# Kernel tuning notes

Measured on AMD Instinct MI355X. Metric: run time of the kernel, lower is better.

## Reference

```python
import jax, jax.numpy as jnp
import numpy as np

B, L, H, V = 64, 2048, 1024, 50257


def setup_inputs() -> dict:
    key = jax.random.key(0)
    ks = jax.random.split(key, 12)
    s = 0.02
    return {
        "input_seq": jax.random.randint(ks[0], (B,), 0, V),
        "encoder_outputs": jax.random.normal(ks[1], (L, B, H), jnp.float32),
        "h0": jax.random.normal(ks[2], (1, B, H), jnp.float32),
        "c0": jax.random.normal(ks[3], (1, B, H), jnp.float32),
        "emb": jax.random.normal(ks[4], (V, H), jnp.float32) * s,
        "W_ih": jax.random.normal(ks[5], (4 * H, H), jnp.float32) * s,
        "W_hh": jax.random.normal(ks[6], (4 * H, H), jnp.float32) * s,
        "b_ih": jnp.zeros((4 * H,), jnp.float32),
        "b_hh": jnp.zeros((4 * H,), jnp.float32),
        "W_concat": jax.random.normal(ks[7], (H, 2 * H), jnp.float32) * s,
        "b_concat": jnp.zeros((H,), jnp.float32),
        "W_out": jax.random.normal(ks[8], (V, H), jnp.float32) * s,
        "b_out": jnp.zeros((V,), jnp.float32),
    }


def reference(input_seq, encoder_outputs, h0, c0, emb, W_ih, W_hh, b_ih, b_hh,
              W_concat, b_concat, W_out, b_out):
    # Embedding lookup (dropout is identity at eval)
    x = emb[input_seq]                      # [B, H]
    h, c = h0[0], c0[0]                     # [B, H] each (n_layers == 1)

    # Single LSTM step, PyTorch gate order (i, f, g, o)
    gates = x @ W_ih.T + b_ih + h @ W_hh.T + b_hh   # [B, 4H]
    i, f, g, o = jnp.split(gates, 4, axis=-1)
    i, f, o = jax.nn.sigmoid(i), jax.nn.sigmoid(f), jax.nn.sigmoid(o)
    g = jnp.tanh(g)
    c1 = f * c + i * g
    h1 = o * jnp.tanh(c1)                   # rnn_output, [B, H]

    # Luong 'dot' attention: replaces the per-(b,i) python double loop
    energies = jnp.einsum('bh,lbh->bl', h1, encoder_outputs)   # [B, L]
    attn = jax.nn.softmax(energies, axis=1)                    # [B, L]
    context = jnp.einsum('bl,lbh->bh', attn, encoder_outputs)  # [B, H]

    concat_out = jnp.tanh(jnp.concatenate([h1, context], axis=1) @ W_concat.T + b_concat)
    output = concat_out @ W_out.T + b_out                      # [B, V]

    return output, h1[None], c1[None], attn[:, None, :]
```

## Files before the change

kernel.cpp:

```cpp
#include <hip/hip_runtime.h>
#include <math.h>

#define B 64
#define Lw 2048
#define Hd 1024
#define Vd 50257

#define WS_XHB    0
#define WS_CATB   98304
#define WS_ENERGY 163840
#define WS_PART   294912
#define WS_CONC   2408448

#define OUT_H1   3216448
#define OUT_C1   3281984
#define OUT_ATTN 3347520

#define NCHUNK 32
#define LCHUNK 64
#define PSTRIDE 1032

typedef __bf16 bf16x8 __attribute__((ext_vector_type(8)));
typedef float f32x4 __attribute__((ext_vector_type(4)));

__device__ __forceinline__ float sigm(float x) { return 1.f / (1.f + expf(-x)); }

#define CVT8(dst, w0, w1)                                            \
    dst[0] = (__bf16)w0.x; dst[1] = (__bf16)w0.y;                    \
    dst[2] = (__bf16)w0.z; dst[3] = (__bf16)w0.w;                    \
    dst[4] = (__bf16)w1.x; dst[5] = (__bf16)w1.y;                    \
    dst[6] = (__bf16)w1.z; dst[7] = (__bf16)w1.w;

__global__ void k_embed(const int* __restrict__ seq, const float* __restrict__ emb,
                        const float* __restrict__ h0, __bf16* __restrict__ xhb)
{
    int b = blockIdx.x;
    int t = threadIdx.x;
    int tok = seq[b];
    float4 xv = *(const float4*)(emb + (size_t)tok * Hd + t * 4);
    float4 hv = *(const float4*)(h0 + (size_t)b * Hd + t * 4);
    int kb = t >> 1, ko = (t & 1) * 4;
    __bf16* xp = xhb + (size_t)kb * 512 + b * 8 + ko;
    xp[0] = (__bf16)xv.x; xp[1] = (__bf16)xv.y;
    xp[2] = (__bf16)xv.z; xp[3] = (__bf16)xv.w;
    __bf16* hp = xhb + (size_t)(128 + kb) * 512 + b * 8 + ko;
    __bf16* lp = xhb + (size_t)(256 + kb) * 512 + b * 8 + ko;
    float h[4] = {hv.x, hv.y, hv.z, hv.w};
#pragma unroll
    for (int i = 0; i < 4; ++i) {
        __bf16 hi = (__bf16)h[i];
        hp[i] = hi;
        lp[i] = (__bf16)(h[i] - (float)hi);
    }
}

__global__ void k_gates_lstm(const __bf16* __restrict__ xhb,
                             const float* __restrict__ W_ih, const float* __restrict__ W_hh,
                             const float* __restrict__ b_ih, const float* __restrict__ b_hh,
                             const float* __restrict__ c0,
                             float* __restrict__ h1o, float* __restrict__ c1o,
                             __bf16* __restrict__ catb)
{
    __shared__ float lds[8][64][20];
    __shared__ float gsum[16][66];
    int wave = threadIdx.x >> 6, lane = threadIdx.x & 63;
    int hh0 = blockIdx.x * 4;
    int rloc = lane & 15;
    int wrow = (rloc >> 2) * Hd + hh0 + (rloc & 3);
    int kq = lane >> 4;
    int isH = wave >> 2;
    int kbase = (wave & 3) * 256;

    const float* wp = (isH ? W_hh : W_ih) + (size_t)wrow * Hd + kbase + kq * 8;
    const __bf16* apx = xhb + rloc * 8;

    f32x4 acc[4] = {{0.f,0.f,0.f,0.f},{0.f,0.f,0.f,0.f},
                    {0.f,0.f,0.f,0.f},{0.f,0.f,0.f,0.f}};

    if (!isH) {
#pragma unroll 4
        for (int k0 = 0; k0 < 256; k0 += 32) {
            float4 w0 = *(const float4*)(wp + k0);
            float4 w1 = *(const float4*)(wp + k0 + 4);
            bf16x8 bf; CVT8(bf, w0, w1);
            int kb = ((kbase + k0) >> 3) + kq;
#pragma unroll
            for (int mt = 0; mt < 4; ++mt) {
                bf16x8 a = *(const bf16x8*)(apx + (size_t)kb * 512 + mt * 128);
                acc[mt] = __builtin_amdgcn_mfma_f32_16x16x32_bf16(a, bf, acc[mt], 0, 0, 0);
            }
        }
    } else {
#pragma unroll 2
        for (int k0 = 0; k0 < 256; k0 += 32) {
            float4 w0 = *(const float4*)(wp + k0);
            float4 w1 = *(const float4*)(wp + k0 + 4);
            bf16x8 bhi, blo;
            float wf[8] = {w0.x, w0.y, w0.z, w0.w, w1.x, w1.y, w1.z, w1.w};
#pragma unroll
            for (int i = 0; i < 8; ++i) {
                __bf16 hi = (__bf16)wf[i];
                bhi[i] = hi;
                blo[i] = (__bf16)(wf[i] - (float)hi);
            }
            int kb = ((kbase + k0) >> 3) + kq;
#pragma unroll
            for (int mt = 0; mt < 4; ++mt) {
                bf16x8 ahi = *(const bf16x8*)(apx + (size_t)(128 + kb) * 512 + mt * 128);
                bf16x8 alo = *(const bf16x8*)(apx + (size_t)(256 + kb) * 512 + mt * 128);
                acc[mt] = __builtin_amdgcn_mfma_f32_16x16x32_bf16(ahi, bhi, acc[mt], 0, 0, 0);
                acc[mt] = __builtin_amdgcn_mfma_f32_16x16x32_bf16(ahi, blo, acc[mt], 0, 0, 0);
                acc[mt] = __builtin_amdgcn_mfma_f32_16x16x32_bf16(alo, bhi, acc[mt], 0, 0, 0);
            }
        }
    }

#pragma unroll
    for (int mt = 0; mt < 4; ++mt)
        *(f32x4*)&lds[wave][lane][mt * 4] = acc[mt];
    __syncthreads();

    if (wave < 4) {
        int mt = wave;
        float bv = b_ih[wrow] + b_hh[wrow];
#pragma unroll
        for (int r = 0; r < 4; ++r) {
            float s = 0.f;
#pragma unroll
            for (int w = 0; w < 8; ++w) s += lds[w][lane][mt * 4 + r];
            int m = mt * 16 + kq * 4 + r;
            gsum[rloc][m] = s + bv;
        }
    }
    __syncthreads();

    int t = threadIdx.x;
    if (t < 256) {
        int b = t & 63, hl = t >> 6;
        int hh = hh0 + hl;
        float gi = gsum[0 + hl][b];
        float gf = gsum[4 + hl][b];
        float gg = gsum[8 + hl][b];
        float go = gsum[12 + hl][b];
        float c  = c0[(size_t)b * Hd + hh];
        float c1 = sigm(gf) * c + sigm(gi) * tanhf(gg);
        float h1 = sigm(go) * tanhf(c1);
        h1o[(size_t)b * Hd + hh] = h1;
        c1o[(size_t)b * Hd + hh] = c1;
        catb[(size_t)(hh >> 3) * 512 + b * 8 + (hh & 7)] = (__bf16)h1;
    }
}

__global__ void k_attn_part(const float* __restrict__ enc, const float* __restrict__ h1,
                            float* __restrict__ energy, float* __restrict__ part)
{
    int chunk = blockIdx.x, b = blockIdx.y;
    int wave = threadIdx.x >> 6, lane = threadIdx.x & 63;

    float4 qv[4], ctx[4];
#pragma unroll
    for (int q = 0; q < 4; ++q) {
        qv[q] = *(const float4*)(h1 + (size_t)b * Hd + q * 256 + lane * 4);
        ctx[q] = make_float4(0.f, 0.f, 0.f, 0.f);
    }
    float m = -INFINITY, s = 0.f;

    int l0 = chunk * LCHUNK + wave * 2;
    const float* ep0 = enc + ((size_t)l0 * B + b) * Hd + lane * 4;
    const float* ep1 = ep0 + (size_t)B * Hd;
    float4 ev0[4], ev1[4];
#pragma unroll
    for (int q = 0; q < 4; ++q) {
        ev0[q] = *(const float4*)(ep0 + q * 256);
        ev1[q] = *(const float4*)(ep1 + q * 256);
    }

    for (int i = 0; i < LCHUNK / 8; ++i) {
        int l = chunk * LCHUNK + i * 8 + wave * 2;
        int ln = (i < LCHUNK / 8 - 1) ? (l + 8) : l;
        const float* np0 = enc + ((size_t)ln * B + b) * Hd + lane * 4;
        const float* np1 = np0 + (size_t)B * Hd;
        float4 nv0[4], nv1[4];
#pragma unroll
        for (int q = 0; q < 4; ++q) {
            nv0[q] = *(const float4*)(np0 + q * 256);
            nv1[q] = *(const float4*)(np1 + q * 256);
        }

        float d0 = 0.f, d1 = 0.f;
#pragma unroll
        for (int q = 0; q < 4; ++q) {
            d0 += ev0[q].x * qv[q].x + ev0[q].y * qv[q].y
                + ev0[q].z * qv[q].z + ev0[q].w * qv[q].w;
            d1 += ev1[q].x * qv[q].x + ev1[q].y * qv[q].y
                + ev1[q].z * qv[q].z + ev1[q].w * qv[q].w;
        }
#pragma unroll
        for (int off = 32; off >= 1; off >>= 1) {
            d0 += __shfl_xor(d0, off);
            d1 += __shfl_xor(d1, off);
        }
        if (lane == 0) {
            energy[(size_t)b * Lw + l] = d0;
            energy[(size_t)b * Lw + l + 1] = d1;
        }

        float mn = fmaxf(d0, d1);
        if (mn > m) {
            float sc = expf(m - mn);
            s *= sc;
#pragma unroll
            for (int q = 0; q < 4; ++q) {
                ctx[q].x *= sc; ctx[q].y *= sc; ctx[q].z *= sc; ctx[q].w *= sc;
            }
            m = mn;
        }
        float w0 = expf(d0 - m), w1 = expf(d1 - m);
        s += w0 + w1;
#pragma unroll
        for (int q = 0; q < 4; ++q) {
            ctx[q].x += w0 * ev0[q].x + w1 * ev1[q].x;
            ctx[q].y += w0 * ev0[q].y + w1 * ev1[q].y;
            ctx[q].z += w0 * ev0[q].z + w1 * ev1[q].z;
            ctx[q].w += w0 * ev0[q].w + w1 * ev1[q].w;
        }
#pragma unroll
        for (int q = 0; q < 4; ++q) { ev0[q] = nv0[q]; ev1[q] = nv1[q]; }
    }

    __shared__ float lctx[4][Hd];
    __shared__ float lms[4][2];
#pragma unroll
    for (int q = 0; q < 4; ++q)
        *(float4*)(&lctx[wave][q * 256 + lane * 4]) = ctx[q];
    if (lane == 0) { lms[wave][0] = m; lms[wave][1] = s; }
    __syncthreads();

    float mb = fmaxf(fmaxf(lms[0][0], lms[1][0]), fmaxf(lms[2][0], lms[3][0]));
    float sc0 = expf(lms[0][0] - mb), sc1 = expf(lms[1][0] - mb);
    float sc2 = expf(lms[2][0] - mb), sc3 = expf(lms[3][0] - mb);
    float sb = lms[0][1] * sc0 + lms[1][1] * sc1 + lms[2][1] * sc2 + lms[3][1] * sc3;

    int t = threadIdx.x;
    float* pb = part + (size_t)(chunk * B + b) * PSTRIDE;
    float4 a0 = *(float4*)(&lctx[0][t * 4]);
    float4 a1 = *(float4*)(&lctx[1][t * 4]);
    float4 a2 = *(float4*)(&lctx[2][t * 4]);
    float4 a3 = *(float4*)(&lctx[3][t * 4]);
    float4 v;
    v.x = a0.x * sc0 + a1.x * sc1 + a2.x * sc2 + a3.x * sc3;
    v.y = a0.y * sc0 + a1.y * sc1 + a2.y * sc2 + a3.y * sc3;
    v.z = a0.z * sc0 + a1.z * sc1 + a2.z * sc2 + a3.z * sc3;
    v.w = a0.w * sc0 + a1.w * sc1 + a2.w * sc2 + a3.w * sc3;
    *(float4*)(pb + t * 4) = v;
    if (t == 0) { pb[1024] = mb; pb[1025] = sb; }
}

__global__ void k_attn_combine(const float* __restrict__ part,
                               const float* __restrict__ energy,
                               __bf16* __restrict__ catb, float* __restrict__ attn)
{
    int b = blockIdx.x, t = threadIdx.x;
    float m = -INFINITY;
#pragma unroll
    for (int c = 0; c < NCHUNK; ++c)
        m = fmaxf(m, part[(size_t)(c * B + b) * PSTRIDE + 1024]);
    float s = 0.f, scl[NCHUNK];
#pragma unroll
    for (int c = 0; c < NCHUNK; ++c) {
        const float* pb = part + (size_t)(c * B + b) * PSTRIDE;
        scl[c] = expf(pb[1024] - m);
        s += pb[1025] * scl[c];
    }
    float4 v = make_float4(0.f, 0.f, 0.f, 0.f);
#pragma unroll
    for (int c = 0; c < NCHUNK; ++c) {
        float4 p = *(const float4*)(part + (size_t)(c * B + b) * PSTRIDE + t * 4);
        v.x += p.x * scl[c]; v.y += p.y * scl[c]; v.z += p.z * scl[c]; v.w += p.w * scl[c];
    }
    float inv = 1.f / s;
    v.x *= inv; v.y *= inv; v.z *= inv; v.w *= inv;
    int k = 1024 + t * 4;
    __bf16* cp = catb + (size_t)(k >> 3) * 512 + b * 8 + (k & 7);
    cp[0] = (__bf16)v.x; cp[1] = (__bf16)v.y;
    cp[2] = (__bf16)v.z; cp[3] = (__bf16)v.w;

#pragma unroll
    for (int j = 0; j < 8; ++j) {
        int l = t + j * 256;
        attn[(size_t)b * Lw + l] = expf(energy[(size_t)b * Lw + l] - m) * inv;
    }
}

__global__ void k_concat_mfma(const __bf16* __restrict__ catb,
                              const float* __restrict__ W, const float* __restrict__ bias,
                              __bf16* __restrict__ conc)
{
    __shared__ float lds[8][64][20];
    int wave = threadIdx.x >> 6, lane = threadIdx.x & 63;
    int n0 = blockIdx.x * 16;
    int nl = n0 + (lane & 15);
    int kq = lane >> 4;
    int kbase = wave * 256;

    const float* wp = W + (size_t)nl * (2 * Hd) + kbase + kq * 8;
    const __bf16* ap = catb + (lane & 15) * 8;

    f32x4 acc[4] = {{0.f,0.f,0.f,0.f},{0.f,0.f,0.f,0.f},
                    {0.f,0.f,0.f,0.f},{0.f,0.f,0.f,0.f}};

#pragma unroll 4
    for (int k0 = 0; k0 < 256; k0 += 32) {
        float4 w0 = *(const float4*)(wp + k0);
        float4 w1 = *(const float4*)(wp + k0 + 4);
        bf16x8 bf; CVT8(bf, w0, w1);
        int kb = ((kbase + k0) >> 3) + kq;
#pragma unroll
        for (int mt = 0; mt < 4; ++mt) {
            bf16x8 a = *(const bf16x8*)(ap + (size_t)kb * 512 + mt * 128);
            acc[mt] = __builtin_amdgcn_mfma_f32_16x16x32_bf16(a, bf, acc[mt], 0, 0, 0);
        }
    }

#pragma unroll
    for (int mt = 0; mt < 4; ++mt)
        *(f32x4*)&lds[wave][lane][mt * 4] = acc[mt];
    __syncthreads();

    if (wave < 4) {
        int mt = wave;
        float bv = bias[nl];
#pragma unroll
        for (int r = 0; r < 4; ++r) {
            float s = 0.f;
#pragma unroll
            for (int w = 0; w < 8; ++w) s += lds[w][lane][mt * 4 + r];
            int m = mt * 16 + kq * 4 + r;
            conc[(size_t)(nl >> 3) * 512 + m * 8 + (nl & 7)] = (__bf16)tanhf(s + bv);
        }
    }
}

__global__ void k_vocab_mfma(const __bf16* __restrict__ apack,
                             const float* __restrict__ W,
                             const float* __restrict__ bias,
                             float* __restrict__ out)
{
    int wave = threadIdx.x >> 6;
    int lane = threadIdx.x & 63;
    int n0 = (blockIdx.x * 4 + wave) * 16;
    if (n0 > Vd - 16) n0 = Vd - 16;

    int nl = n0 + (lane & 15);
    int kq = lane >> 4;
    const float* wp = W + (size_t)nl * Hd + kq * 8;
    const __bf16* ap = apack + (size_t)(lane & 15) * 8;

    f32x4 acc[4] = {{0.f,0.f,0.f,0.f},{0.f,0.f,0.f,0.f},
                    {0.f,0.f,0.f,0.f},{0.f,0.f,0.f,0.f}};

    float4 c0 = *(const float4*)(wp + 0);
    float4 c1 = *(const float4*)(wp + 4);
    float4 c2 = *(const float4*)(wp + 32);
    float4 c3 = *(const float4*)(wp + 36);

#pragma unroll 2
    for (int k0 = 0; k0 < Hd; k0 += 64) {
        int kn = (k0 + 64 < Hd) ? (k0 + 64) : k0;
        float4 p0 = *(const float4*)(wp + kn);
        float4 p1 = *(const float4*)(wp + kn + 4);
        float4 p2 = *(const float4*)(wp + kn + 32);
        float4 p3 = *(const float4*)(wp + kn + 36);

        bf16x8 bf0; CVT8(bf0, c0, c1);
        bf16x8 bf1; CVT8(bf1, c2, c3);
        int kb0 = (k0 >> 3) + kq, kb1 = kb0 + 4;
#pragma unroll
        for (int mt = 0; mt < 4; ++mt) {
            bf16x8 a0 = *(const bf16x8*)(ap + (size_t)kb0 * 512 + mt * 128);
            acc[mt] = __builtin_amdgcn_mfma_f32_16x16x32_bf16(a0, bf0, acc[mt], 0, 0, 0);
        }
#pragma unroll
        for (int mt = 0; mt < 4; ++mt) {
            bf16x8 a1 = *(const bf16x8*)(ap + (size_t)kb1 * 512 + mt * 128);
            acc[mt] = __builtin_amdgcn_mfma_f32_16x16x32_bf16(a1, bf1, acc[mt], 0, 0, 0);
        }
        c0 = p0; c1 = p1; c2 = p2; c3 = p3;
    }

    float bv = bias[nl];
#pragma unroll
    for (int mt = 0; mt < 4; ++mt)
#pragma unroll
        for (int r = 0; r < 4; ++r) {
            int m = mt * 16 + (lane >> 4) * 4 + r;
            out[(size_t)m * Vd + nl] = acc[mt][r] + bv;
        }
}

extern "C" void kernel_launch(void* const* d_in, const int* in_sizes, int n_in,
                              void* d_out, int out_size, void* d_ws, size_t ws_size,
                              hipStream_t stream)
{
    const int*   seq    = (const int*)d_in[0];
    const float* enc    = (const float*)d_in[1];
    const float* h0     = (const float*)d_in[2];
    const float* c0     = (const float*)d_in[3];
    const float* emb    = (const float*)d_in[4];
    const float* W_ih   = (const float*)d_in[5];
    const float* W_hh   = (const float*)d_in[6];
    const float* b_ih   = (const float*)d_in[7];
    const float* b_hh   = (const float*)d_in[8];
    const float* W_cat  = (const float*)d_in[9];
    const float* b_cat  = (const float*)d_in[10];
    const float* W_out  = (const float*)d_in[11];
    const float* b_out  = (const float*)d_in[12];
    float* out = (float*)d_out;
    float* ws  = (float*)d_ws;

    __bf16* xhb    = (__bf16*)(ws + WS_XHB);
    __bf16* catb   = (__bf16*)(ws + WS_CATB);
    float*  energy = ws + WS_ENERGY;
    float*  part   = ws + WS_PART;
    __bf16* conc   = (__bf16*)(ws + WS_CONC);

    k_embed<<<B, 256, 0, stream>>>(seq, emb, h0, xhb);
    k_gates_lstm<<<256, 512, 0, stream>>>(xhb, W_ih, W_hh, b_ih, b_hh, c0,
                                          out + OUT_H1, out + OUT_C1, catb);
    k_attn_part<<<dim3(NCHUNK, B), 256, 0, stream>>>(enc, out + OUT_H1, energy, part);
    k_attn_combine<<<B, 256, 0, stream>>>(part, energy, catb, out + OUT_ATTN);
    k_concat_mfma<<<64, 512, 0, stream>>>(catb, W_cat, b_cat, conc);
    k_vocab_mfma<<<786, 256, 0, stream>>>(conc, W_out, b_out, out);
}
```

Before: 232.2 us.

## Fuse embedding into LSTM gates, merge attention combine via atomic counter, shrink vocab blocks

Removes the separate embedding kernel: the gates kernel now gathers embedding rows and h0 directly from fp32 and converts or splits them to bf16 in registers. The attention combine kernel is folded into the partial kernel, where the last block per batch row (found with an atomic counter that the gates kernel resets) does the final reduction. The manual register prefetch in the attention loop is dropped, and the vocab GEMM switches to 128-thread blocks with twice as many blocks. This saves two launches, but the gates kernel now repeats conversions and global gathers, and dropping the prefetch may expose more memory latency.

Measured after the change: 781.3 us. 237% more time.

```diff
diff --git a/kernel.cpp b/kernel.cpp
--- a/kernel.cpp
+++ b/kernel.cpp
@@ -6,11 +6,11 @@
 #define Hd 1024
 #define Vd 50257
 
-#define WS_XHB    0
-#define WS_CATB   98304
-#define WS_ENERGY 163840
-#define WS_PART   294912
-#define WS_CONC   2408448
+#define WS_CATB   0
+#define WS_ENERGY 65536
+#define WS_PART   196608
+#define WS_CNT    2310144
+#define WS_CONC   2310272
 
 #define OUT_H1   3216448
 #define OUT_C1   3281984
@@ -31,38 +31,19 @@
     dst[4] = (__bf16)w1.x; dst[5] = (__bf16)w1.y;                    \
     dst[6] = (__bf16)w1.z; dst[7] = (__bf16)w1.w;
 
-__global__ void k_embed(const int* __restrict__ seq, const float* __restrict__ emb,
-                        const float* __restrict__ h0, __bf16* __restrict__ xhb)
-{
-    int b = blockIdx.x;
-    int t = threadIdx.x;
-    int tok = seq[b];
-    float4 xv = *(const float4*)(emb + (size_t)tok * Hd + t * 4);
-    float4 hv = *(const float4*)(h0 + (size_t)b * Hd + t * 4);
-    int kb = t >> 1, ko = (t & 1) * 4;
-    __bf16* xp = xhb + (size_t)kb * 512 + b * 8 + ko;
-    xp[0] = (__bf16)xv.x; xp[1] = (__bf16)xv.y;
-    xp[2] = (__bf16)xv.z; xp[3] = (__bf16)xv.w;
-    __bf16* hp = xhb + (size_t)(128 + kb) * 512 + b * 8 + ko;
-    __bf16* lp = xhb + (size_t)(256 + kb) * 512 + b * 8 + ko;
-    float h[4] = {hv.x, hv.y, hv.z, hv.w};
-#pragma unroll
-    for (int i = 0; i < 4; ++i) {
-        __bf16 hi = (__bf16)h[i];
-        hp[i] = hi;
-        lp[i] = (__bf16)(h[i] - (float)hi);
-    }
-}
-
-__global__ void k_gates_lstm(const __bf16* __restrict__ xhb,
+__global__ void k_gates_lstm(const int* __restrict__ seq,
+                             const float* __restrict__ emb, const float* __restrict__ h0,
                              const float* __restrict__ W_ih, const float* __restrict__ W_hh,
                              const float* __restrict__ b_ih, const float* __restrict__ b_hh,
                              const float* __restrict__ c0,
                              float* __restrict__ h1o, float* __restrict__ c1o,
-                             __bf16* __restrict__ catb)
+                             __bf16* __restrict__ catb, int* __restrict__ cnt)
 {
     __shared__ float lds[8][64][20];
     __shared__ float gsum[16][66];
+
+    if (blockIdx.x == 0 && threadIdx.x < 64) cnt[threadIdx.x] = 0;
+
     int wave = threadIdx.x >> 6, lane = threadIdx.x & 63;
     int hh0 = blockIdx.x * 4;
     int rloc = lane & 15;
@@ -72,22 +53,26 @@
     int kbase = (wave & 3) * 256;
 
     const float* wp = (isH ? W_hh : W_ih) + (size_t)wrow * Hd + kbase + kq * 8;
-    const __bf16* apx = xhb + rloc * 8;
 
     f32x4 acc[4] = {{0.f,0.f,0.f,0.f},{0.f,0.f,0.f,0.f},
                     {0.f,0.f,0.f,0.f},{0.f,0.f,0.f,0.f}};
 
     if (!isH) {
-#pragma unroll 4
+        int tok[4];
+#pragma unroll
+        for (int mt = 0; mt < 4; ++mt) tok[mt] = seq[mt * 16 + rloc];
+#pragma unroll 2
         for (int k0 = 0; k0 < 256; k0 += 32) {
             float4 w0 = *(const float4*)(wp + k0);
             float4 w1 = *(const float4*)(wp + k0 + 4);
             bf16x8 bf; CVT8(bf, w0, w1);
-            int kb = ((kbase + k0) >> 3) + kq;
 #pragma unroll
             for (int mt = 0; mt < 4; ++mt) {
-                bf16x8 a = *(const bf16x8*)(apx + (size_t)kb * 512 + mt * 128);
-                acc[mt] = __builtin_amdgcn_mfma_f32_16x16x32_bf16(a, bf, acc[mt], 0, 0, 0);
+                const float* xp = emb + (size_t)tok[mt] * Hd + kbase + k0 + kq * 8;
+                float4 a0 = *(const float4*)xp;
+                float4 a1 = *(const float4*)(xp + 4);
+                bf16x8 af; CVT8(af, a0, a1);
+                acc[mt] = __builtin_amdgcn_mfma_f32_16x16x32_bf16(af, bf, acc[mt], 0, 0, 0);
             }
         }
     } else {
@@ -96,18 +81,28 @@
             float4 w0 = *(const float4*)(wp + k0);
             float4 w1 = *(const float4*)(wp + k0 + 4);
             bf16x8 bhi, blo;
-            float wf[8] = {w0.x, w0.y, w0.z, w0.w, w1.x, w1.y, w1.z, w1.w};
-#pragma unroll
-            for (int i = 0; i < 8; ++i) {
-                __bf16 hi = (__bf16)wf[i];
-                bhi[i] = hi;
-                blo[i] = (__bf16)(wf[i] - (float)hi);
+            {
+                float wf[8] = {w0.x, w0.y, w0.z, w0.w, w1.x, w1.y, w1.z, w1.w};
+#pragma unroll
+                for (int i = 0; i < 8; ++i) {
+                    __bf16 hi = (__bf16)wf[i];
+                    bhi[i] = hi;
+                    blo[i] = (__bf16)(wf[i] - (float)hi);
+                }
             }
-            int kb = ((kbase + k0) >> 3) + kq;
 #pragma unroll
             for (int mt = 0; mt < 4; ++mt) {
-                bf16x8 ahi = *(const bf16x8*)(apx + (size_t)(128 + kb) * 512 + mt * 128);
-                bf16x8 alo = *(const bf16x8*)(apx + (size_t)(256 + kb) * 512 + mt * 128);
+                const float* hp = h0 + (size_t)(mt * 16 + rloc) * Hd + kbase + k0 + kq * 8;
+                float4 a0 = *(const float4*)hp;
+                float4 a1 = *(const float4*)(hp + 4);
+                float hf[8] = {a0.x, a0.y, a0.z, a0.w, a1.x, a1.y, a1.z, a1.w};
+                bf16x8 ahi, alo;
+#pragma unroll
+                for (int i = 0; i < 8; ++i) {
+                    __bf16 hi = (__bf16)hf[i];
+                    ahi[i] = hi;
+                    alo[i] = (__bf16)(hf[i] - (float)hi);
+                }
                 acc[mt] = __builtin_amdgcn_mfma_f32_16x16x32_bf16(ahi, bhi, acc[mt], 0, 0, 0);
                 acc[mt] = __builtin_amdgcn_mfma_f32_16x16x32_bf16(ahi, blo, acc[mt], 0, 0, 0);
                 acc[mt] = __builtin_amdgcn_mfma_f32_16x16x32_bf16(alo, bhi, acc[mt], 0, 0, 0);
@@ -152,7 +147,9 @@
 }
 
 __global__ void k_attn_part(const float* __restrict__ enc, const float* __restrict__ h1,
-                            float* __restrict__ energy, float* __restrict__ part)
+                            float* __restrict__ energy, float* __restrict__ part,
+                            int* __restrict__ cnt, __bf16* __restrict__ catb,
+                            float* __restrict__ attn)
 {
     int chunk = blockIdx.x, b = blockIdx.y;
     int wave = threadIdx.x >> 6, lane = threadIdx.x & 63;
@@ -165,28 +162,16 @@
     }
     float m = -INFINITY, s = 0.f;
 
-    int l0 = chunk * LCHUNK + wave * 2;
-    const float* ep0 = enc + ((size_t)l0 * B + b) * Hd + lane * 4;
-    const float* ep1 = ep0 + (size_t)B * Hd;
-    float4 ev0[4], ev1[4];
-#pragma unroll
-    for (int q = 0; q < 4; ++q) {
-        ev0[q] = *(const float4*)(ep0 + q * 256);
-        ev1[q] = *(const float4*)(ep1 + q * 256);
-    }
-
     for (int i = 0; i < LCHUNK / 8; ++i) {
         int l = chunk * LCHUNK + i * 8 + wave * 2;
-        int ln = (i < LCHUNK / 8 - 1) ? (l + 8) : l;
-        const float* np0 = enc + ((size_t)ln * B + b) * Hd + lane * 4;
-        const float* np1 = np0 + (size_t)B * Hd;
-        float4 nv0[4], nv1[4];
+        const float* ep0 = enc + ((size_t)l * B + b) * Hd + lane * 4;
+        const float* ep1 = ep0 + (size_t)B * Hd;
+        float4 ev0[4], ev1[4];
 #pragma unroll
         for (int q = 0; q < 4; ++q) {
-            nv0[q] = *(const float4*)(np0 + q * 256);
-            nv1[q] = *(const float4*)(np1 + q * 256);
-        }
-
+            ev0[q] = *(const float4*)(ep0 + q * 256);
+            ev1[q] = *(const float4*)(ep1 + q * 256);
+        }
         float d0 = 0.f, d1 = 0.f;
 #pragma unroll
         for (int q = 0; q < 4; ++q) {
@@ -224,12 +209,11 @@
             ctx[q].z += w0 * ev0[q].z + w1 * ev1[q].z;
             ctx[q].w += w0 * ev0[q].w + w1 * ev1[q].w;
         }
-#pragma unroll
-        for (int q = 0; q < 4; ++q) { ev0[q] = nv0[q]; ev1[q] = nv1[q]; }
     }
 
     __shared__ float lctx[4][Hd];
     __shared__ float lms[4][2];
+    __shared__ int isLast;
 #pragma unroll
     for (int q = 0; q < 4; ++q)
         *(float4*)(&lctx[wave][q * 256 + lane * 4]) = ctx[q];
@@ -254,41 +238,45 @@
     v.w = a0.w * sc0 + a1.w * sc1 + a2.w * sc2 + a3.w * sc3;
     *(float4*)(pb + t * 4) = v;
     if (t == 0) { pb[1024] = mb; pb[1025] = sb; }
-}
-
-__global__ void k_attn_combine(const float* __restrict__ part,
-                               const float* __restrict__ energy,
-                               __bf16* __restrict__ catb, float* __restrict__ attn)
-{
-    int b = blockIdx.x, t = threadIdx.x;
-    float m = -INFINITY;
+
+    __threadfence();
+    if (t == 0) {
+        int old = atomicAdd(&cnt[b], 1);
+        isLast = (old == NCHUNK - 1);
+    }
+    __syncthreads();
+    if (!isLast) return;
+    __threadfence();
+
+    float M = -INFINITY;
 #pragma unroll
     for (int c = 0; c < NCHUNK; ++c)
-        m = fmaxf(m, part[(size_t)(c * B + b) * PSTRIDE + 1024]);
-    float s = 0.f, scl[NCHUNK];
+        M = fmaxf(M, part[(size_t)(c * B + b) * PSTRIDE + 1024]);
+    float S = 0.f, scl[NCHUNK];
 #pragma unroll
     for (int c = 0; c < NCHUNK; ++c) {
-        const float* pb = part + (size_t)(c * B + b) * PSTRIDE;
-        scl[c] = expf(pb[1024] - m);
-        s += pb[1025] * scl[c];
-    }
-    float4 v = make_float4(0.f, 0.f, 0.f, 0.f);
+        const float* pc = part + (size_t)(c * B + b) * PSTRIDE;
+        scl[c] = expf(pc[1024] - M);
+        S += pc[1025] * scl[c];
+    }
+    float4 cv = make_float4(0.f, 0.f, 0.f, 0.f);
 #pragma unroll
     for (int c = 0; c < NCHUNK; ++c) {
         float4 p = *(const float4*)(part + (size_t)(c * B + b) * PSTRIDE + t * 4);
-        v.x += p.x * scl[c]; v.y += p.y * scl[c]; v.z += p.z * scl[c]; v.w += p.w * scl[c];
-    }
-    float inv = 1.f / s;
-    v.x *= inv; v.y *= inv; v.z *= inv; v.w *= inv;
+        cv.x += p.x * scl[c]; cv.y += p.y * scl[c];
+        cv.z += p.z * scl[c]; cv.w += p.w * scl[c];
+    }
+    float inv = 1.f / S;
+    cv.x *= inv; cv.y *= inv; cv.z *= inv; cv.w *= inv;
     int k = 1024 + t * 4;
     __bf16* cp = catb + (size_t)(k >> 3) * 512 + b * 8 + (k & 7);
-    cp[0] = (__bf16)v.x; cp[1] = (__bf16)v.y;
-    cp[2] = (__bf16)v.z; cp[3] = (__bf16)v.w;
+    cp[0] = (__bf16)cv.x; cp[1] = (__bf16)cv.y;
+    cp[2] = (__bf16)cv.z; cp[3] = (__bf16)cv.w;
 
 #pragma unroll
     for (int j = 0; j < 8; ++j) {
         int l = t + j * 256;
-        attn[(size_t)b * Lw + l] = expf(energy[(size_t)b * Lw + l] - m) * inv;
+        attn[(size_t)b * Lw + l] = expf(energy[(size_t)b * Lw + l] - M) * inv;
     }
 }
 
@@ -348,7 +336,7 @@
 {
     int wave = threadIdx.x >> 6;
     int lane = threadIdx.x & 63;
-    int n0 = (blockIdx.x * 4 + wave) * 16;
+    int n0 = (blockIdx.x * 2 + wave) * 16;
     if (n0 > Vd - 16) n0 = Vd - 16;
 
     int nl = n0 + (lane & 15);
@@ -418,17 +406,16 @@
     float* out = (float*)d_out;
     float* ws  = (float*)d_ws;
 
-    __bf16* xhb    = (__bf16*)(ws + WS_XHB);
     __bf16* catb   = (__bf16*)(ws + WS_CATB);
     float*  energy = ws + WS_ENERGY;
     float*  part   = ws + WS_PART;
+    int*    cnt    = (int*)(ws + WS_CNT);
     __bf16* conc   = (__bf16*)(ws + WS_CONC);
 
-    k_embed<<<B, 256, 0, stream>>>(seq, emb, h0, xhb);
-    k_gates_lstm<<<256, 512, 0, stream>>>(xhb, W_ih, W_hh, b_ih, b_hh, c0,
-                                          out + OUT_H1, out + OUT_C1, catb);
-    k_attn_part<<<dim3(NCHUNK, B), 256, 0, stream>>>(enc, out + OUT_H1, energy, part);
-    k_attn_combine<<<B, 256, 0, stream>>>(part, energy, catb, out + OUT_ATTN);
+    k_gates_lstm<<<256, 512, 0, stream>>>(seq, emb, h0, W_ih, W_hh, b_ih, b_hh, c0,
+                                          out + OUT_H1, out + OUT_C1, catb, cnt);
+    k_attn_part<<<dim3(NCHUNK, B), 256, 0, stream>>>(enc, out + OUT_H1, energy, part,
+                                                     cnt, catb, out + OUT_ATTN);
     k_concat_mfma<<<64, 512, 0, stream>>>(catb, W_cat, b_cat, conc);
-    k_vocab_mfma<<<786, 256, 0, stream>>>(conc, W_out, b_out, out);
+    k_vocab_mfma<<<1571, 128, 0, stream>>>(conc, W_out, b_out, out);
 }
```
